# Performance work log

Hardware: AMD Instinct MI355X
Metric: run time of the kernel (lower is better)

## Reference

```python
import jax, jax.numpy as jnp
import numpy as np

B, S, D, H = 2, 2048, 1024, 16
HD = D // H
MEAN = -1.0e9
STD = abs(MEAN) * 0.1  # min(foresight=0.5, 0.1)


def setup_inputs() -> dict:
    key = jax.random.key(0)
    ks = jax.random.split(key, 8)
    scale = 0.02
    return {
        "inputs": jax.random.normal(ks[0], (B, S, D), dtype=jnp.float32),
        "Wq": jax.random.normal(ks[1], (D, D), dtype=jnp.float32) * scale,
        "bq": jax.random.normal(ks[2], (D,), dtype=jnp.float32) * scale,
        "Wk": jax.random.normal(ks[3], (D, D), dtype=jnp.float32) * scale,
        "bk": jax.random.normal(ks[4], (D,), dtype=jnp.float32) * scale,
        "Wv": jax.random.normal(ks[5], (D, D), dtype=jnp.float32) * scale,
        "Wo": jax.random.normal(ks[6], (D, D), dtype=jnp.float32) * scale,
        "bo": jax.random.normal(ks[7], (D,), dtype=jnp.float32) * scale,
    }


def reference(inputs, Wq, bq, Wk, bk, Wv, Wo, bo):
    # projections (weights stored [in, out])
    q = (inputs @ Wq + bq).reshape(B, S, H, HD).transpose(0, 2, 1, 3)  # [B,H,S,HD]
    k = (inputs @ Wk + bk).reshape(B, S, H, HD).transpose(0, 2, 1, 3)
    v = (inputs @ Wv).reshape(B, S, H, HD).transpose(0, 2, 1, 3)

    scores = jnp.einsum("bhid,bhjd->bhij", q, k) / jnp.sqrt(jnp.float32(HD))

    # ALiBi bias as written: slopes[h] * positions[j], broadcast over query index i
    slopes = 2.0 ** (-8.0 * jnp.arange(1, H + 1, dtype=jnp.float32) / H)
    positions = jnp.arange(S, dtype=jnp.float32)
    scores = scores - slopes[None, :, None, None] * positions[None, None, None, :]

    # causal stochastic soft mask: scatter_add with identity index == elementwise add
    causal = jnp.tril(jnp.ones((S, S), dtype=jnp.float32))  # [S,S]
    soft_mask = MEAN + STD * jax.random.normal(jax.random.key(42), (B, H, S, S), dtype=jnp.float32)
    scores = scores + soft_mask * (1.0 - causal)[None, None]

    weights = jax.nn.softmax(scores, axis=-1)
    out = jnp.einsum("bhij,bhjd->bhid", weights, v)  # [B,H,S,HD]
    out = out.transpose(0, 2, 1, 3).reshape(B, S, D)
    return out @ Wo + bo
```

## Files before the change

kernel.cpp:

```cpp
#include <hip/hip_runtime.h>
#include <math.h>

#define BB 2
#define SS 2048
#define DD 1024
#define HH 16
#define HDD 64

typedef __attribute__((ext_vector_type(4))) short short4v;
typedef __attribute__((ext_vector_type(8))) short short8v;
typedef __attribute__((ext_vector_type(4))) unsigned short ushort4v;
typedef __attribute__((ext_vector_type(8))) unsigned short ushort8v;
typedef __attribute__((ext_vector_type(2))) unsigned int uint2v;
typedef __attribute__((ext_vector_type(4))) float f32x4;

__device__ __forceinline__ unsigned short f2bf(float f) {
    union { float f; unsigned u; } v; v.f = f;
    return (unsigned short)((v.u + 0x7FFFu + ((v.u >> 16) & 1u)) >> 16);
}
__device__ __forceinline__ float bf2f(unsigned short b) {
    union { unsigned u; float f; } v; v.u = (unsigned)b << 16;
    return v.f;
}
__device__ __forceinline__ unsigned cvtpk(float lo, float hi) {
    unsigned r;
    asm("v_cvt_pk_bf16_f32 %0, %1, %2" : "=v"(r) : "v"(lo), "v"(hi));
    return r;
}

__device__ __forceinline__ void gload_lds16(const void* g, void* l) {
    __builtin_amdgcn_global_load_lds(
        (const __attribute__((address_space(1))) void*)g,
        (__attribute__((address_space(3))) void*)l, 16, 0, 0);
}

__global__ __launch_bounds__(256) void convert_x(const float* __restrict__ x,
                                                 unsigned short* __restrict__ xb) {
    const size_t i = ((size_t)blockIdx.x * 256 + threadIdx.x) * 8;
    const float4 a = *(const float4*)&x[i];
    const float4 b = *(const float4*)&x[i + 4];
    ushort8v o;
    o[0] = f2bf(a.x); o[1] = f2bf(a.y); o[2] = f2bf(a.z); o[3] = f2bf(a.w);
    o[4] = f2bf(b.x); o[5] = f2bf(b.y); o[6] = f2bf(b.z); o[7] = f2bf(b.w);
    *(ushort8v*)&xb[i] = o;
}

__global__ __launch_bounds__(256) void transpose_w(
    const float* __restrict__ W0, const float* __restrict__ W1,
    const float* __restrict__ W2, const float* __restrict__ W3,
    unsigned short* __restrict__ T0, unsigned short* __restrict__ T1,
    unsigned short* __restrict__ T2, unsigned short* __restrict__ T3) {
    const int z = blockIdx.z;
    const float* W = z == 0 ? W0 : z == 1 ? W1 : z == 2 ? W2 : W3;
    unsigned short* T = z == 0 ? T0 : z == 1 ? T1 : z == 2 ? T2 : T3;
    const int k0 = blockIdx.x * 64, n0 = blockIdx.y * 64;
    const int tid = threadIdx.x;
    __shared__ unsigned short tt[64][65];
    const int rr = tid >> 4, cc = (tid & 15) * 4;
    #pragma unroll
    for (int it = 0; it < 4; ++it) {
        const int r = it * 16 + rr;
        const float4 v = *(const float4*)&W[(size_t)(k0 + r) * DD + n0 + cc];
        tt[r][cc + 0] = f2bf(v.x); tt[r][cc + 1] = f2bf(v.y);
        tt[r][cc + 2] = f2bf(v.z); tt[r][cc + 3] = f2bf(v.w);
    }
    __syncthreads();
    #pragma unroll
    for (int it = 0; it < 4; ++it) {
        const int n = it * 16 + rr;
        ushort4v o;
        o[0] = tt[cc + 0][n]; o[1] = tt[cc + 1][n];
        o[2] = tt[cc + 2][n]; o[3] = tt[cc + 3][n];
        *(ushort4v*)&T[(size_t)(n0 + n) * DD + k0 + cc] = o;
    }
}

template<int MODE, int NF>
__global__ __launch_bounds__(256) void gemm_bf16(
    const unsigned short* __restrict__ A,
    const unsigned short* __restrict__ Wt0, const unsigned short* __restrict__ Wt1,
    const unsigned short* __restrict__ Wt2,
    const float* __restrict__ bias0, const float* __restrict__ bias1,
    unsigned short* __restrict__ O0, unsigned short* __restrict__ O1,
    unsigned short* __restrict__ O2,
    float* __restrict__ Of, const float* __restrict__ biasf)
{
    constexpr int BN = NF * 32;
    const int tid = threadIdx.x;
    const int w = tid >> 6, lane = tid & 63;
    const int wm = w >> 1, wn = w & 1;
    const int c = lane & 15, g = lane >> 4;
    const int m0 = blockIdx.x * 128;

    const unsigned short* Wsel;
    int nn0, mat = 0;
    if (MODE == 0) {
        const int by = blockIdx.y;
        mat = by >> 3;
        nn0 = (by & 7) * 128;
        Wsel = mat == 0 ? Wt0 : mat == 1 ? Wt1 : Wt2;
    } else {
        nn0 = blockIdx.y * BN;
        Wsel = Wt0;
    }

    __shared__ alignas(16) unsigned short As[128 * 32];
    __shared__ alignas(16) unsigned short Bs[BN * 32];

    f32x4 acc[4][NF];
    #pragma unroll
    for (int mf = 0; mf < 4; ++mf)
        #pragma unroll
        for (int nf = 0; nf < NF; ++nf) acc[mf][nf] = f32x4{0.f, 0.f, 0.f, 0.f};

    const int lr = lane >> 2;
    const int lc8 = (lane & 3) * 8;

    for (int kt = 0; kt < DD; kt += 32) {
        #pragma unroll
        for (int i = 0; i < 2; ++i) {
            const int ii = w * 2 + i;
            gload_lds16(&A[(size_t)(m0 + ii * 16 + lr) * DD + kt + lc8], &As[ii * 512]);
        }
        if (NF == 4) {
            #pragma unroll
            for (int i = 0; i < 2; ++i) {
                const int ii = w * 2 + i;
                gload_lds16(&Wsel[(size_t)(nn0 + ii * 16 + lr) * DD + kt + lc8], &Bs[ii * 512]);
            }
        } else {
            gload_lds16(&Wsel[(size_t)(nn0 + w * 16 + lr) * DD + kt + lc8], &Bs[w * 512]);
        }
        __syncthreads();

        short8v a[4], bfr[NF];
        #pragma unroll
        for (int mf = 0; mf < 4; ++mf)
            a[mf] = *(const short8v*)&As[(wm * 64 + mf * 16 + c) * 32 + 8 * g];
        #pragma unroll
        for (int nf = 0; nf < NF; ++nf)
            bfr[nf] = *(const short8v*)&Bs[(wn * (NF * 16) + nf * 16 + c) * 32 + 8 * g];
        #pragma unroll
        for (int mf = 0; mf < 4; ++mf)
            #pragma unroll
            for (int nf = 0; nf < NF; ++nf)
                acc[mf][nf] = __builtin_amdgcn_mfma_f32_16x16x32_bf16(
                    a[mf], bfr[nf], acc[mf][nf], 0, 0, 0);
        __syncthreads();
    }

    if (MODE == 0) {
        unsigned short* Odst = mat == 0 ? O0 : mat == 1 ? O1 : O2;
        const float* bp = mat == 0 ? bias0 : mat == 1 ? bias1 : nullptr;
        #pragma unroll
        for (int nf = 0; nf < NF; ++nf) {
            const int nl = nn0 + wn * 64 + nf * 16 + c;
            const int h = nl >> 6, hd = nl & 63;
            const float bv = bp ? bp[nl] : 0.0f;
            #pragma unroll
            for (int mf = 0; mf < 4; ++mf)
                #pragma unroll
                for (int r = 0; r < 4; ++r) {
                    const int m = m0 + wm * 64 + mf * 16 + 4 * g + r;
                    const int b_ = m >> 11, s_ = m & (SS - 1);
                    Odst[(((size_t)(b_ * HH + h) * SS) + s_) * HDD + hd] =
                        f2bf(acc[mf][nf][r] + bv);
                }
        }
    } else {
        #pragma unroll
        for (int nf = 0; nf < NF; ++nf) {
            const int n = nn0 + wn * (NF * 16) + nf * 16 + c;
            const float bv = biasf[n];
            #pragma unroll
            for (int mf = 0; mf < 4; ++mf)
                #pragma unroll
                for (int r = 0; r < 4; ++r) {
                    const int m = m0 + wm * 64 + mf * 16 + 4 * g + r;
                    Of[(size_t)m * DD + n] = acc[mf][nf][r] + bv;
                }
        }
    }
}

#define LDST 76

__global__ __launch_bounds__(256) void attn_mfma_bf16(
    const unsigned short* __restrict__ Q, const unsigned short* __restrict__ K,
    const unsigned short* __restrict__ V,
    unsigned short* __restrict__ Opart, float* __restrict__ Lpart)
{
    const int t    = blockIdx.x;
    const int qt   = 31 - (t >> 6);
    const int bh   = t & 31;
    const int half = (t >> 5) & 1;
    const int h    = bh & 15;
    const int tid  = threadIdx.x;
    const int w    = tid >> 6;
    const int lane = tid & 63;
    const int c    = lane & 15;
    const int g    = lane >> 4;

    const int h0    = (qt + 2) >> 1;
    const int kt_lo = half ? h0 : 0;
    const int kt_hi = half ? (qt + 1) : h0;

    __shared__ unsigned short Ks[64][LDST];
    __shared__ unsigned short Vt[64][LDST];
    __shared__ unsigned int   Pw4[4][16][36];

    const float LOG2E = 1.44269504f;
    const float slope = exp2f(-0.5f * (float)(h + 1)) * LOG2E;
    const float scale = 0.125f * LOG2E;
    float srl[4];
    #pragma unroll
    for (int r = 0; r < 4; ++r) srl[r] = slope * (float)r;

    const int srow = tid >> 2;
    const int sc   = tid & 3;
    const int scol = sc * 16;
    const int vcol = (srow + scol) & 63;

    const size_t baseQ = ((size_t)bh * SS + (size_t)qt * 64) * HDD;

    short8v qf[2];
    {
        const size_t qrow = baseQ + (size_t)(w * 16 + c) * HDD;
        qf[0] = *(const short8v*)&Q[qrow + 8 * g];
        qf[1] = *(const short8v*)&Q[qrow + 32 + 8 * g];
    }

    float l_ = 0.0f;
    f32x4 o_[4];
    #pragma unroll
    for (int ds = 0; ds < 4; ++ds) o_[ds] = f32x4{0.f, 0.f, 0.f, 0.f};

    const int ig = qt * 64 + w * 16 + c;

    for (int kt = kt_lo; kt < kt_hi; ++kt) {
        __syncthreads();
        const size_t baseK = ((size_t)bh * SS + (size_t)kt * 64) * HDD;
        {
            const size_t rb = baseK + (size_t)srow * HDD + scol;
            const ushort8v k0 = *(const ushort8v*)&K[rb];
            const ushort8v k1 = *(const ushort8v*)&K[rb + 8];
            ushort4v tv;
            tv[0]=k0[0]; tv[1]=k0[1]; tv[2]=k0[2]; tv[3]=k0[3];
            *(ushort4v*)&Ks[srow][scol]      = tv;
            tv[0]=k0[4]; tv[1]=k0[5]; tv[2]=k0[6]; tv[3]=k0[7];
            *(ushort4v*)&Ks[srow][scol + 4]  = tv;
            tv[0]=k1[0]; tv[1]=k1[1]; tv[2]=k1[2]; tv[3]=k1[3];
            *(ushort4v*)&Ks[srow][scol + 8]  = tv;
            tv[0]=k1[4]; tv[1]=k1[5]; tv[2]=k1[6]; tv[3]=k1[7];
            *(ushort4v*)&Ks[srow][scol + 12] = tv;
            const ushort8v v0 = *(const ushort8v*)&V[rb];
            const ushort8v v1 = *(const ushort8v*)&V[rb + 8];
            #pragma unroll
            for (int t2 = 0; t2 < 8; ++t2) {
                Vt[scol + t2][vcol]     = v0[t2];
                Vt[scol + 8 + t2][vcol] = v1[t2];
            }
        }
        __syncthreads();

        f32x4 acc[4];
        #pragma unroll
        for (int js = 0; js < 4; ++js) {
            f32x4 a = {0.f, 0.f, 0.f, 0.f};
            const int krow = js * 16 + c;
            #pragma unroll
            for (int ks = 0; ks < 2; ++ks) {
                short4v lo = *(const short4v*)&Ks[krow][32 * ks + 8 * g];
                short4v hi = *(const short4v*)&Ks[krow][32 * ks + 8 * g + 4];
                short8v kf = {lo[0], lo[1], lo[2], lo[3], hi[0], hi[1], hi[2], hi[3]};
                a = __builtin_amdgcn_mfma_f32_16x16x32_bf16(kf, qf[ks], a, 0, 0, 0);
            }
            acc[js] = a;
        }

        const bool diag = (kt == qt);
        const int jb0 = kt * 64 + 4 * g;
        #pragma unroll
        for (int js = 0; js < 4; ++js) {
            const float bj = fmaf(-slope, (float)(jb0 + js * 16), -8.0f);
            float p[4];
            #pragma unroll
            for (int r = 0; r < 4; ++r) {
                float val = fmaf(acc[js][r], scale, bj - srl[r]);
                if (diag && (jb0 + js * 16 + r) > ig) val = -1.0e30f;
                p[r] = exp2f(val);
                l_ += p[r];
            }
            Pw4[w][c][js * 8 + 2 * g]     = cvtpk(p[0], p[1]);
            Pw4[w][c][js * 8 + 2 * g + 1] = cvtpk(p[2], p[3]);
        }

        asm volatile("s_waitcnt lgkmcnt(0)" ::: "memory");
        __builtin_amdgcn_sched_barrier(0);

        short8v pf[2];
        #pragma unroll
        for (int ks = 0; ks < 2; ++ks)
            pf[ks] = *(const short8v*)&Pw4[w][c][16 * ks + 4 * g];
        #pragma unroll
        for (int ds = 0; ds < 4; ++ds) {
            const int vrow = ds * 16 + c;
            #pragma unroll
            for (int ks = 0; ks < 2; ++ks) {
                const int cb = (32 * ks + 8 * g + 16 * ds) & 63;
                short4v lo = *(const short4v*)&Vt[vrow][cb];
                short4v hi = *(const short4v*)&Vt[vrow][cb + 4];
                short8v vf = {lo[0], lo[1], lo[2], lo[3], hi[0], hi[1], hi[2], hi[3]};
                o_[ds] = __builtin_amdgcn_mfma_f32_16x16x32_bf16(vf, pf[ks], o_[ds], 0, 0, 0);
            }
        }
    }

    l_ += __shfl_xor(l_, 16, 64);
    l_ += __shfl_xor(l_, 32, 64);

    const int pid = ((bh << 5) | qt) * 2 + half;
    unsigned short* Op = Opart + (size_t)pid * 64 * 64;
    const size_t orow = (size_t)(w * 16 + c) * 64;
    #pragma unroll
    for (int ds = 0; ds < 4; ++ds) {
        uint2v pk;
        pk[0] = cvtpk(o_[ds][0], o_[ds][1]);
        pk[1] = cvtpk(o_[ds][2], o_[ds][3]);
        *(uint2v*)&Op[orow + ds * 16 + 4 * g] = pk;
    }
    if (g == 0) Lpart[pid * 64 + w * 16 + c] = l_;
}

__global__ __launch_bounds__(256) void merge_attn(
    const unsigned short* __restrict__ Opart,
    const float* __restrict__ Lpart,
    unsigned short* __restrict__ Out)
{
    const int item = blockIdx.x;
    const int bh = item >> 5, qt = item & 31;
    const int b = bh >> 4, h = bh & 15;
    const int tid = threadIdx.x;
    const int row = tid >> 2, dg = (tid & 3) * 16;
    const int p0 = item * 2, p1 = p0 + 1;

    const float l1 = Lpart[p0 * 64 + row];
    const float l2 = Lpart[p1 * 64 + row];
    const float inv = 1.0f / (l1 + l2);

    const ushort8v* o1p = (const ushort8v*)&Opart[((size_t)p0 * 64 + row) * 64 + dg];
    const ushort8v* o2p = (const ushort8v*)&Opart[((size_t)p1 * 64 + row) * 64 + dg];
    unsigned short* dst = &Out[((size_t)b * SS + qt * 64 + row) * DD + h * HDD + dg];
    #pragma unroll
    for (int q2 = 0; q2 < 2; ++q2) {
        const ushort8v a = o1p[q2], bb = o2p[q2];
        ushort8v o;
        #pragma unroll
        for (int e = 0; e < 8; ++e)
            o[e] = f2bf((bf2f(a[e]) + bf2f(bb[e])) * inv);
        *(ushort8v*)(dst + q2 * 8) = o;
    }
}

extern "C" void kernel_launch(void* const* d_in, const int* in_sizes, int n_in,
                              void* d_out, int out_size, void* d_ws, size_t ws_size,
                              hipStream_t stream) {
    const float* x  = (const float*)d_in[0];
    const float* Wq = (const float*)d_in[1];
    const float* bq = (const float*)d_in[2];
    const float* Wk = (const float*)d_in[3];
    const float* bk = (const float*)d_in[4];
    const float* Wv = (const float*)d_in[5];
    const float* Wo = (const float*)d_in[6];
    const float* bo = (const float*)d_in[7];

    unsigned short* ws = (unsigned short*)d_ws;
    unsigned short* xb    = ws;
    unsigned short* Wqt   = ws + 4194304;
    unsigned short* Wkt   = ws + 5242880;
    unsigned short* Wvt   = ws + 6291456;
    unsigned short* Wot   = ws + 7340032;
    unsigned short* Qb    = ws + 8388608;
    unsigned short* Kb    = ws + 12582912;
    unsigned short* Vb    = ws + 16777216;
    unsigned short* attnb = ws + 20971520;
    unsigned short* Opart = ws + 25165824;
    float* Lpart = (float*)(ws + 33554432);

    convert_x<<<2048, 256, 0, stream>>>(x, xb);
    transpose_w<<<dim3(16, 16, 4), 256, 0, stream>>>(Wq, Wk, Wv, Wo,
                                                     Wqt, Wkt, Wvt, Wot);

    gemm_bf16<0, 4><<<dim3(32, 24), 256, 0, stream>>>(
        xb, Wqt, Wkt, Wvt, bq, bk, Qb, Kb, Vb, nullptr, nullptr);

    attn_mfma_bf16<<<2048, 256, 0, stream>>>(Qb, Kb, Vb, Opart, Lpart);
    merge_attn<<<1024, 256, 0, stream>>>(Opart, Lpart, attnb);

    gemm_bf16<1, 2><<<dim3(32, 16), 256, 0, stream>>>(
        attnb, Wot, nullptr, nullptr, nullptr, nullptr,
        nullptr, nullptr, nullptr, (float*)d_out, bo);
}
```

Measured before the change: 193.0 us.

## Enlarge attention query tile to 128 rows with 8-wave blocks

The attention kernel now processes 128 query rows per block with 512 threads (8 waves), where it used 64 rows and 4 waves. Each K/V tile staged in shared memory is therefore reused by twice as many query rows, halving global K/V traffic and staging work per query. The causal split between the two halves and the diagonal mask test are reworked for the larger tile, and the merge kernel indexing is updated to match. It also raises wave priority with s_setprio around the MFMA sections. In exchange, blocks are larger and fewer, which may reduce scheduling flexibility and increase the shared-memory footprint per block.

```diff
diff --git a/kernel.cpp b/kernel.cpp
--- a/kernel.cpp
+++ b/kernel.cpp
@@ -185,13 +185,13 @@
 
 #define LDST 76
 
-__global__ __launch_bounds__(256) void attn_mfma_bf16(
+__global__ __launch_bounds__(512) void attn_mfma_bf16(
     const unsigned short* __restrict__ Q, const unsigned short* __restrict__ K,
     const unsigned short* __restrict__ V,
     unsigned short* __restrict__ Opart, float* __restrict__ Lpart)
 {
     const int t    = blockIdx.x;
-    const int qt   = 31 - (t >> 6);
+    const int qt   = 15 - (t >> 6);
     const int bh   = t & 31;
     const int half = (t >> 5) & 1;
     const int h    = bh & 15;
@@ -201,13 +201,12 @@
     const int c    = lane & 15;
     const int g    = lane >> 4;
 
-    const int h0    = (qt + 2) >> 1;
-    const int kt_lo = half ? h0 : 0;
-    const int kt_hi = half ? (qt + 1) : h0;
+    const int kt_lo = half ? (qt + 1) : 0;
+    const int kt_hi = half ? (2 * qt + 2) : (qt + 1);
 
     __shared__ unsigned short Ks[64][LDST];
     __shared__ unsigned short Vt[64][LDST];
-    __shared__ unsigned int   Pw4[4][16][36];
+    __shared__ unsigned int   Pw4[8][16][36];
 
     const float LOG2E = 1.44269504f;
     const float slope = exp2f(-0.5f * (float)(h + 1)) * LOG2E;
@@ -216,12 +215,12 @@
     #pragma unroll
     for (int r = 0; r < 4; ++r) srl[r] = slope * (float)r;
 
-    const int srow = tid >> 2;
-    const int sc   = tid & 3;
-    const int scol = sc * 16;
-    const int vcol = (srow + scol) & 63;
-
-    const size_t baseQ = ((size_t)bh * SS + (size_t)qt * 64) * HDD;
+    const int srow = tid >> 3;
+    const int s8   = tid & 7;
+    const int scol = s8 * 8;
+    const int vcol = (srow + 16 * ((s8 >> 1) & 3)) & 63;
+
+    const size_t baseQ = ((size_t)bh * SS + (size_t)qt * 128) * HDD;
 
     short8v qf[2];
     {
@@ -235,7 +234,7 @@
     #pragma unroll
     for (int ds = 0; ds < 4; ++ds) o_[ds] = f32x4{0.f, 0.f, 0.f, 0.f};
 
-    const int ig = qt * 64 + w * 16 + c;
+    const int ig = qt * 128 + w * 16 + c;
 
     for (int kt = kt_lo; kt < kt_hi; ++kt) {
         __syncthreads();
@@ -243,26 +242,19 @@
         {
             const size_t rb = baseK + (size_t)srow * HDD + scol;
             const ushort8v k0 = *(const ushort8v*)&K[rb];
-            const ushort8v k1 = *(const ushort8v*)&K[rb + 8];
             ushort4v tv;
             tv[0]=k0[0]; tv[1]=k0[1]; tv[2]=k0[2]; tv[3]=k0[3];
-            *(ushort4v*)&Ks[srow][scol]      = tv;
+            *(ushort4v*)&Ks[srow][scol]     = tv;
             tv[0]=k0[4]; tv[1]=k0[5]; tv[2]=k0[6]; tv[3]=k0[7];
-            *(ushort4v*)&Ks[srow][scol + 4]  = tv;
-            tv[0]=k1[0]; tv[1]=k1[1]; tv[2]=k1[2]; tv[3]=k1[3];
-            *(ushort4v*)&Ks[srow][scol + 8]  = tv;
-            tv[0]=k1[4]; tv[1]=k1[5]; tv[2]=k1[6]; tv[3]=k1[7];
-            *(ushort4v*)&Ks[srow][scol + 12] = tv;
+            *(ushort4v*)&Ks[srow][scol + 4] = tv;
             const ushort8v v0 = *(const ushort8v*)&V[rb];
-            const ushort8v v1 = *(const ushort8v*)&V[rb + 8];
-            #pragma unroll
-            for (int t2 = 0; t2 < 8; ++t2) {
-                Vt[scol + t2][vcol]     = v0[t2];
-                Vt[scol + 8 + t2][vcol] = v1[t2];
-            }
+            #pragma unroll
+            for (int t2 = 0; t2 < 8; ++t2)
+                Vt[scol + t2][vcol] = v0[t2];
         }
         __syncthreads();
 
+        __builtin_amdgcn_s_setprio(1);
         f32x4 acc[4];
         #pragma unroll
         for (int js = 0; js < 4; ++js) {
@@ -277,8 +269,9 @@
             }
             acc[js] = a;
         }
-
-        const bool diag = (kt == qt);
+        __builtin_amdgcn_s_setprio(0);
+
+        const bool diag = (kt >= 2 * qt);
         const int jb0 = kt * 64 + 4 * g;
         #pragma unroll
         for (int js = 0; js < 4; ++js) {
@@ -298,6 +291,7 @@
         asm volatile("s_waitcnt lgkmcnt(0)" ::: "memory");
         __builtin_amdgcn_sched_barrier(0);
 
+        __builtin_amdgcn_s_setprio(1);
         short8v pf[2];
         #pragma unroll
         for (int ks = 0; ks < 2; ++ks)
@@ -314,13 +308,14 @@
                 o_[ds] = __builtin_amdgcn_mfma_f32_16x16x32_bf16(vf, pf[ks], o_[ds], 0, 0, 0);
             }
         }
+        __builtin_amdgcn_s_setprio(0);
     }
 
     l_ += __shfl_xor(l_, 16, 64);
     l_ += __shfl_xor(l_, 32, 64);
 
-    const int pid = ((bh << 5) | qt) * 2 + half;
-    unsigned short* Op = Opart + (size_t)pid * 64 * 64;
+    const int pid = ((bh << 4) | qt) * 2 + half;
+    unsigned short* Op = Opart + (size_t)pid * 128 * 64;
     const size_t orow = (size_t)(w * 16 + c) * 64;
     #pragma unroll
     for (int ds = 0; ds < 4; ++ds) {
@@ -329,7 +324,7 @@
         pk[1] = cvtpk(o_[ds][2], o_[ds][3]);
         *(uint2v*)&Op[orow + ds * 16 + 4 * g] = pk;
     }
-    if (g == 0) Lpart[pid * 64 + w * 16 + c] = l_;
+    if (g == 0) Lpart[pid * 128 + w * 16 + c] = l_;
 }
 
 __global__ __launch_bounds__(256) void merge_attn(
@@ -337,20 +332,21 @@
     const float* __restrict__ Lpart,
     unsigned short* __restrict__ Out)
 {
-    const int item = blockIdx.x;
-    const int bh = item >> 5, qt = item & 31;
+    const int item = blockIdx.x >> 1;
+    const int sub  = blockIdx.x & 1;
+    const int bh = item >> 4, qt = item & 15;
     const int b = bh >> 4, h = bh & 15;
     const int tid = threadIdx.x;
-    const int row = tid >> 2, dg = (tid & 3) * 16;
+    const int row = sub * 64 + (tid >> 2), dg = (tid & 3) * 16;
     const int p0 = item * 2, p1 = p0 + 1;
 
-    const float l1 = Lpart[p0 * 64 + row];
-    const float l2 = Lpart[p1 * 64 + row];
+    const float l1 = Lpart[p0 * 128 + row];
+    const float l2 = Lpart[p1 * 128 + row];
     const float inv = 1.0f / (l1 + l2);
 
-    const ushort8v* o1p = (const ushort8v*)&Opart[((size_t)p0 * 64 + row) * 64 + dg];
-    const ushort8v* o2p = (const ushort8v*)&Opart[((size_t)p1 * 64 + row) * 64 + dg];
-    unsigned short* dst = &Out[((size_t)b * SS + qt * 64 + row) * DD + h * HDD + dg];
+    const ushort8v* o1p = (const ushort8v*)&Opart[((size_t)p0 * 128 + row) * 64 + dg];
+    const ushort8v* o2p = (const ushort8v*)&Opart[((size_t)p1 * 128 + row) * 64 + dg];
+    unsigned short* dst = &Out[((size_t)b * SS + qt * 128 + row) * DD + h * HDD + dg];
     #pragma unroll
     for (int q2 = 0; q2 < 2; ++q2) {
         const ushort8v a = o1p[q2], bb = o2p[q2];
@@ -394,7 +390,7 @@
     gemm_bf16<0, 4><<<dim3(32, 24), 256, 0, stream>>>(
         xb, Wqt, Wkt, Wvt, bq, bk, Qb, Kb, Vb, nullptr, nullptr);
 
-    attn_mfma_bf16<<<2048, 256, 0, stream>>>(Qb, Kb, Vb, Opart, Lpart);
+    attn_mfma_bf16<<<1024, 512, 0, stream>>>(Qb, Kb, Vb, Opart, Lpart);
     merge_attn<<<1024, 256, 0, stream>>>(Opart, Lpart, attnb);
 
     gemm_bf16<1, 2><<<dim3(32, 16), 256, 0, stream>>>(
```

Result: no change. 189.7 us (-1.7%).
